# Performance work log

Hardware: AMD Instinct MI355X
Metric: run time of the kernel (lower is better)

Reference implementation:

```python
import jax, jax.numpy as jnp
import numpy as np

B, S, E, H, FF = 4, 2048, 1024, 16, 4096
TD = 32  # transition_dim


def _layer_norm(v, g, b, eps=1e-5):
    m = v.mean(-1, keepdims=True)
    var = ((v - m) ** 2).mean(-1, keepdims=True)
    return (v - m) * jax.lax.rsqrt(var + eps) * g + b


def setup_inputs() -> dict:
    key = jax.random.key(0)
    ks = jax.random.split(key, 8)
    w = 0.02
    return {
        "x": jax.random.normal(ks[0], (B, S, E), dtype=jnp.float32),
        "transition_dim": TD,
        "ln1_g": jnp.ones((E,), jnp.float32),
        "ln1_b": jnp.zeros((E,), jnp.float32),
        "ln2_g": jnp.ones((E,), jnp.float32),
        "ln2_b": jnp.zeros((E,), jnp.float32),
        "w_qkv": jax.random.normal(ks[1], (3 * E, E), jnp.float32) * w,
        "b_qkv": jnp.zeros((3 * E,), jnp.float32),
        "w_o": jax.random.normal(ks[2], (E, E), jnp.float32) * w,
        "b_o": jnp.zeros((E,), jnp.float32),
        "w_fc1": jax.random.normal(ks[3], (FF, E), jnp.float32) * w,
        "b_fc1": jnp.zeros((FF,), jnp.float32),
        "w_fc2": jax.random.normal(ks[4], (E, FF), jnp.float32) * w,
        "b_fc2": jnp.zeros((E,), jnp.float32),
    }


def reference(x, transition_dim, ln1_g, ln1_b, ln2_g, ln2_b, w_qkv, b_qkv,
              w_o, b_o, w_fc1, b_fc1, w_fc2, b_fc2):
    Bx, Sx, Ex = x.shape
    Dh = Ex // H
    xn = _layer_norm(x, ln1_g, ln1_b)
    qkv = xn @ w_qkv.T + b_qkv                      # [B,S,3E]
    q, k, v = jnp.split(qkv, 3, axis=-1)
    def heads(t):
        return t.reshape(Bx, Sx, H, Dh).transpose(0, 2, 1, 3)  # [B,H,S,Dh]
    q, k, v = heads(q), heads(k), heads(v)
    scores = jnp.einsum("bhqd,bhkd->bhqk", q, k) / np.sqrt(Dh).astype(np.float32)
    # custom mask: causal (j > i) OR periodic value-column (j % TD == TD-1) blocked
    i = jnp.arange(Sx)
    mask = (i[None, :] > i[:, None]) | ((i[None, :] % transition_dim) == transition_dim - 1)
    scores = jnp.where(mask[None, None], -jnp.inf, scores)
    p = jax.nn.softmax(scores, axis=-1)
    attn = jnp.einsum("bhqk,bhkd->bhqd", p, v)
    attn = attn.transpose(0, 2, 1, 3).reshape(Bx, Sx, Ex)
    attn = attn @ w_o.T + b_o
    x = x + attn
    h = _layer_norm(x, ln2_g, ln2_b)
    h = jax.nn.gelu(h @ w_fc1.T + b_fc1, approximate=False) @ w_fc2.T + b_fc2
    return x + h
```

## Files before the change

kernel.cpp:

```cpp
#include <hip/hip_runtime.h>
#include <hip/hip_bf16.h>

typedef unsigned short u16;
typedef unsigned int u32;
typedef short bf16x8 __attribute__((ext_vector_type(8)));
typedef float f32x4 __attribute__((ext_vector_type(4)));
typedef float f32x16 __attribute__((ext_vector_type(16)));

#define B_ 4
#define S_ 2048
#define E_ 1024
#define H_ 16
#define FF_ 4096
#define M_ 8192

__device__ __forceinline__ u16 f2bf(float f) {
    u32 u = __float_as_uint(f);
    u32 r = (u + 0x7FFFu + ((u >> 16) & 1u)) >> 16;
    return (u16)r;
}
__device__ __forceinline__ float bf2f(u16 v) {
    return __uint_as_float(((u32)v) << 16);
}
__device__ __forceinline__ u32 cvtpk(float lo, float hi) {
    u32 r;
    asm("v_cvt_pk_bf16_f32 %0, %1, %2" : "=v"(r) : "v"(lo), "v"(hi));
    return r;
}
__device__ __forceinline__ void pswap(u32& a, u32& b) {
    asm("v_permlane32_swap_b32 %0, %1" : "+v"(a), "+v"(b));
}
__device__ __forceinline__ void gload16(const void* g, void* l) {
    __builtin_amdgcn_global_load_lds(
        (__attribute__((address_space(1))) void*)g,
        (__attribute__((address_space(3))) void*)l, 16, 0, 0);
}
__device__ __forceinline__ float gelu_f(float v) {
    float y = 0.79788456f * (v + 0.044715f * v * v * v);
    float t = __builtin_amdgcn_exp2f(2.88539008f * y);
    float th = 1.0f - 2.0f / (t + 1.0f);
    return 0.5f * v * (1.0f + th);
}

__global__ __launch_bounds__(256) void cvt4_kernel(const float* __restrict__ s0, u16* __restrict__ d0,
                                                   const float* __restrict__ s1, u16* __restrict__ d1,
                                                   const float* __restrict__ s2, u16* __restrict__ d2,
                                                   const float* __restrict__ s3, u16* __restrict__ d3) {
    int blk = blockIdx.x;
    const float* s; u16* d; int base;
    if (blk < 3072)      { s = s0; d = d0; base = blk; }
    else if (blk < 4096) { s = s1; d = d1; base = blk - 3072; }
    else if (blk < 8192) { s = s2; d = d2; base = blk - 4096; }
    else                 { s = s3; d = d3; base = blk - 8192; }
    int i = base * 256 + threadIdx.x;
    float4 v = ((const float4*)s)[i];
    ushort4 o;
    o.x = f2bf(v.x); o.y = f2bf(v.y); o.z = f2bf(v.z); o.w = f2bf(v.w);
    ((ushort4*)d)[i] = o;
}

__global__ __launch_bounds__(256) void vtrans_kernel(const u16* __restrict__ qkv,
                                                     u16* __restrict__ vt) {
    __shared__ u16 tile[64 * 67];
    int t = threadIdx.x;
    int st = blockIdx.x;
    int bh = blockIdx.y;
    int b = bh >> 4, h = bh & 15;
    int s0 = st * 64;
    int r = t >> 3, c0 = (t & 7) * 8;
#pragma unroll
    for (int half = 0; half < 2; half++) {
        int rr = r + half * 32;
        const u16* src = qkv + (size_t)(b * S_ + s0 + rr) * 3072 + 2048 + h * 64 + c0;
        uint4 v = *(const uint4*)src;
        u16* pv = (u16*)&v;
#pragma unroll
        for (int e = 0; e < 8; e++) tile[(c0 + e) * 67 + rr] = pv[e];
    }
    __syncthreads();
    int d = t >> 2, ch = t & 3;
    u16 buf[16];
#pragma unroll
    for (int j = 0; j < 16; j++) buf[j] = tile[d * 67 + ch * 16 + j];
    u16* dst = vt + ((size_t)bh * 64 + d) * 2048 + s0 + ch * 16;
    *(uint4*)dst = *(uint4*)&buf[0];
    *(uint4*)(dst + 8) = *(uint4*)&buf[8];
}

__global__ __launch_bounds__(256) void ln_kernel(const float* __restrict__ x,
                                                 const float* __restrict__ g,
                                                 const float* __restrict__ bb,
                                                 u16* __restrict__ out) {
    int row = blockIdx.x;
    int t = threadIdx.x;
    const float4* xr = (const float4*)(x + (size_t)row * E_);
    float4 v = xr[t];
    float s = v.x + v.y + v.z + v.w;
    float sq = v.x * v.x + v.y * v.y + v.z * v.z + v.w * v.w;
    for (int o = 1; o < 64; o <<= 1) {
        s += __shfl_xor(s, o, 64);
        sq += __shfl_xor(sq, o, 64);
    }
    __shared__ float ss[4], sqs[4];
    int w = t >> 6, l = t & 63;
    if (l == 0) { ss[w] = s; sqs[w] = sq; }
    __syncthreads();
    s = ss[0] + ss[1] + ss[2] + ss[3];
    sq = sqs[0] + sqs[1] + sqs[2] + sqs[3];
    float mean = s * (1.0f / E_);
    float var = sq * (1.0f / E_) - mean * mean;
    float rstd = rsqrtf(var + 1e-5f);
    float4 gv = ((const float4*)g)[t];
    float4 bv = ((const float4*)bb)[t];
    ushort4 o4;
    o4.x = f2bf((v.x - mean) * rstd * gv.x + bv.x);
    o4.y = f2bf((v.y - mean) * rstd * gv.y + bv.y);
    o4.z = f2bf((v.z - mean) * rstd * gv.z + bv.z);
    o4.w = f2bf((v.w - mean) * rstd * gv.w + bv.w);
    ((ushort4*)(out + (size_t)row * E_))[t] = o4;
}

__global__ __launch_bounds__(256) void ln_bf16_kernel(const u16* __restrict__ x,
                                                      const float* __restrict__ g,
                                                      const float* __restrict__ bb,
                                                      u16* __restrict__ out) {
    int row = blockIdx.x;
    int t = threadIdx.x;
    ushort4 xv = ((const ushort4*)(x + (size_t)row * E_))[t];
    float v0 = bf2f(xv.x), v1 = bf2f(xv.y), v2 = bf2f(xv.z), v3 = bf2f(xv.w);
    float s = v0 + v1 + v2 + v3;
    float sq = v0 * v0 + v1 * v1 + v2 * v2 + v3 * v3;
    for (int o = 1; o < 64; o <<= 1) {
        s += __shfl_xor(s, o, 64);
        sq += __shfl_xor(sq, o, 64);
    }
    __shared__ float ss[4], sqs[4];
    int w = t >> 6, l = t & 63;
    if (l == 0) { ss[w] = s; sqs[w] = sq; }
    __syncthreads();
    s = ss[0] + ss[1] + ss[2] + ss[3];
    sq = sqs[0] + sqs[1] + sqs[2] + sqs[3];
    float mean = s * (1.0f / E_);
    float var = sq * (1.0f / E_) - mean * mean;
    float rstd = rsqrtf(var + 1e-5f);
    float4 gv = ((const float4*)g)[t];
    float4 bv = ((const float4*)bb)[t];
    ushort4 o4;
    o4.x = f2bf((v0 - mean) * rstd * gv.x + bv.x);
    o4.y = f2bf((v1 - mean) * rstd * gv.y + bv.y);
    o4.z = f2bf((v2 - mean) * rstd * gv.z + bv.z);
    o4.w = f2bf((v3 - mean) * rstd * gv.w + bv.w);
    ((ushort4*)(out + (size_t)row * E_))[t] = o4;
}

template <int EPI>
__global__ __launch_bounds__(512) void gemm256m(const u16* __restrict__ A,
                                                const u16* __restrict__ Bt,
                                                const float* __restrict__ bias,
                                                void* __restrict__ outp,
                                                int N, int K) {
    __shared__ u16 ldsA[2 * 2 * 8192];
    __shared__ u16 ldsB[2 * 2 * 8192];
    int t = threadIdx.x;
    int wid = t >> 6, l = t & 63, l15 = l & 15, hi4 = l >> 4;
    int wm = wid >> 2, wn = wid & 3;

    int nwg = gridDim.x;
    int flat = blockIdx.x;
    int swz = (flat & 7) * (nwg >> 3) + (flat >> 3);
    int nx = N >> 8;
    int nxs = nx >> 2;
    int sid = swz >> 4, wi = swz & 15;
    int sidm = sid / nxs, sidn = sid % nxs;
    int m0 = (sidm * 4 + (wi >> 2)) * 256;
    int n0 = (sidn * 4 + (wi & 3)) * 256;
    const size_t Kb = (size_t)K * 2;

    f32x4 acc[8][4];
    f32x4 zf = {0.f, 0.f, 0.f, 0.f};
#pragma unroll
    for (int i = 0; i < 8; i++)
#pragma unroll
        for (int j = 0; j < 4; j++) acc[i][j] = zf;

    auto stageA = [&](int buf, int h, int k0) {
#pragma unroll
        for (int rr = 0; rr < 2; ++rr) {
            int o = t * 16 + rr * 8192;
            int lr = o >> 7;
            int gch = ((o >> 4) & 7) ^ (lr & 7);
            int grow = m0 + (lr >> 6) * 128 + h * 64 + (lr & 63);
            gload16((const char*)A + (size_t)grow * Kb + k0 * 2 + gch * 16,
                    (char*)ldsA + (buf * 2 + h) * 16384 + o);
        }
    };
    auto stageB = [&](int buf, int h, int k0) {
#pragma unroll
        for (int rr = 0; rr < 2; ++rr) {
            int o = t * 16 + rr * 8192;
            int lr = o >> 7;
            int gch = ((o >> 4) & 7) ^ (lr & 7);
            int grow = n0 + (lr >> 5) * 64 + h * 32 + (lr & 31);
            gload16((const char*)Bt + (size_t)grow * Kb + k0 * 2 + gch * 16,
                    (char*)ldsB + (buf * 2 + h) * 16384 + o);
        }
    };

    auto readA = [&](int bq, int mh, bf16x8 (&af)[4][2]) {
#pragma unroll
        for (int mi = 0; mi < 4; mi++)
#pragma unroll
            for (int ks = 0; ks < 2; ks++) {
                int lr = wm * 64 + mi * 16 + l15;
                int ob = lr * 128 + ks * 64 + hi4 * 16;
                af[mi][ks] = *(const bf16x8*)((const char*)ldsA +
                             (bq * 2 + mh) * 16384 + (ob ^ ((lr & 7) << 4)));
            }
    };
    auto readB = [&](int bq, int nh, bf16x8 (&bfr)[2][2]) {
#pragma unroll
        for (int nq = 0; nq < 2; nq++)
#pragma unroll
            for (int ks = 0; ks < 2; ks++) {
                int lr = wn * 32 + nq * 16 + l15;
                int ob = lr * 128 + ks * 64 + hi4 * 16;
                bfr[nq][ks] = *(const bf16x8*)((const char*)ldsB +
                              (bq * 2 + nh) * 16384 + (ob ^ ((lr & 7) << 4)));
            }
    };
    auto mma = [&](bf16x8 (&af)[4][2], bf16x8 (&bfr)[2][2], int mh, int nh) {
#pragma unroll
        for (int mi = 0; mi < 4; mi++)
#pragma unroll
            for (int nq = 0; nq < 2; nq++)
#pragma unroll
                for (int ks = 0; ks < 2; ks++)
                    acc[mh * 4 + mi][nh * 2 + nq] =
                        __builtin_amdgcn_mfma_f32_16x16x32_bf16(
                            af[mi][ks], bfr[nq][ks], acc[mh * 4 + mi][nh * 2 + nq], 0, 0, 0);
    };

#define GWAIT(N)                                            \
    asm volatile("s_waitcnt vmcnt(" #N ")" ::: "memory");   \
    __builtin_amdgcn_sched_barrier(0);
#define PH_MID                                              \
    __builtin_amdgcn_s_barrier();                           \
    asm volatile("s_waitcnt lgkmcnt(0)" ::: "memory");      \
    __builtin_amdgcn_sched_barrier(0);                      \
    __builtin_amdgcn_s_setprio(1);
#define PH_END                                              \
    __builtin_amdgcn_s_setprio(0);                          \
    __builtin_amdgcn_s_barrier();

    int ITERS = K >> 7;
    stageB(0, 0, 0); stageB(0, 1, 0); stageA(0, 0, 0); stageA(0, 1, 0);
    stageB(1, 0, 64); stageB(1, 1, 64); stageA(1, 0, 64);
    GWAIT(6);
    __builtin_amdgcn_s_barrier();
    for (int s = 0; s < ITERS; ++s) {
        int k1 = (2 * s + 1) << 6;
        int k2 = (2 * s + 2) << 6; if (k2 >= K) k2 = 0;
        int k3 = (2 * s + 3) << 6; if (k3 >= K) k3 = 0;
        bf16x8 af[4][2], b0[2][2], b1[2][2];
        readA(0, 0, af); readB(0, 0, b0); readB(0, 1, b1);
        stageA(1, 1, k1);
        PH_MID; mma(af, b0, 0, 0); mma(af, b1, 0, 1); PH_END;
        readA(0, 1, af);
        stageB(0, 0, k2); stageB(0, 1, k2); stageA(0, 0, k2);
        PH_MID; mma(af, b0, 1, 0); mma(af, b1, 1, 1);
        __builtin_amdgcn_s_setprio(0);
        GWAIT(8);
        __builtin_amdgcn_s_barrier();
        readA(1, 0, af); readB(1, 0, b0); readB(1, 1, b1);
        stageA(0, 1, k2);
        PH_MID; mma(af, b0, 0, 0); mma(af, b1, 0, 1);
        __builtin_amdgcn_s_setprio(0);
        GWAIT(8);
        __builtin_amdgcn_s_barrier();
        readA(1, 1, af);
        stageB(1, 0, k3); stageB(1, 1, k3); stageA(1, 0, k3);
        GWAIT(6);
        PH_MID; mma(af, b0, 1, 0); mma(af, b1, 1, 1); PH_END;
    }
    GWAIT(0);
    __builtin_amdgcn_s_barrier();
#undef GWAIT
#undef PH_MID
#undef PH_END

    float bias_v[4];
#pragma unroll
    for (int nf = 0; nf < 4; nf++) bias_v[nf] = bias[n0 + wn * 64 + nf * 16 + l15];

    u16* myl = (wid < 4 ? ldsA : ldsB) + (wid & 3) * 8192;
#pragma unroll
    for (int mf = 0; mf < 8; mf++)
#pragma unroll
        for (int nf = 0; nf < 4; nf++)
#pragma unroll
            for (int j = 0; j < 4; j++) {
                int row = mf * 16 + hi4 * 4 + j;
                int col = nf * 16 + l15;
                float v = acc[mf][nf][j] + bias_v[nf];
                if (EPI == 2) v = gelu_f(v);
                int chunk = ((col >> 3) + (row >> 2)) & 7;
                myl[row * 64 + chunk * 8 + (col & 7)] = f2bf(v);
            }
    u16* out16 = (u16*)outp;
#pragma unroll
    for (int pass = 0; pass < 16; ++pass) {
        int row = pass * 8 + (l >> 3);
        int chunk = ((l & 7) + (row >> 2)) & 7;
        uint4 d = *(const uint4*)&myl[row * 64 + chunk * 8];
        int grow = m0 + wm * 128 + row;
        int gcol = n0 + wn * 64 + (l & 7) * 8;
        *(uint4*)&out16[(size_t)grow * N + gcol] = d;
    }
}

template <int EPI>
__global__ __launch_bounds__(512) void gemm256n128(const u16* __restrict__ A,
                                                   const u16* __restrict__ Bt,
                                                   const float* __restrict__ bias,
                                                   void* __restrict__ outp,
                                                   const void* __restrict__ residp,
                                                   int N, int K) {
    __shared__ u16 ldsA[2 * 2 * 8192];
    __shared__ u16 ldsB[2 * 8192];
    int t = threadIdx.x;
    int wid = t >> 6, l = t & 63, l15 = l & 15, hi4 = l >> 4;
    int wm = wid >> 2, wn = wid & 3;

    int nwg = gridDim.x;
    int flat = blockIdx.x;
    int swz = (flat & 7) * (nwg >> 3) + (flat >> 3);
    int nx = N >> 7;
    int nxs = nx >> 2;
    int sid = swz >> 4, wi = swz & 15;
    int sidm = sid / nxs, sidn = sid % nxs;
    int m0 = (sidm * 4 + (wi >> 2)) * 256;
    int n0 = (sidn * 4 + (wi & 3)) * 128;
    const size_t Kb = (size_t)K * 2;

    f32x4 acc[8][2];
    f32x4 zf = {0.f, 0.f, 0.f, 0.f};
#pragma unroll
    for (int i = 0; i < 8; i++)
#pragma unroll
        for (int j = 0; j < 2; j++) acc[i][j] = zf;

    auto stageA = [&](int buf, int h, int k0) {
#pragma unroll
        for (int rr = 0; rr < 2; ++rr) {
            int o = t * 16 + rr * 8192;
            int lr = o >> 7;
            int gch = ((o >> 4) & 7) ^ (lr & 7);
            int grow = m0 + (lr >> 6) * 128 + h * 64 + (lr & 63);
            gload16((const char*)A + (size_t)grow * Kb + k0 * 2 + gch * 16,
                    (char*)ldsA + (buf * 2 + h) * 16384 + o);
        }
    };
    auto stageB = [&](int buf, int k0) {
#pragma unroll
        for (int rr = 0; rr < 2; ++rr) {
            int o = t * 16 + rr * 8192;
            int lr = o >> 7;
            int gch = ((o >> 4) & 7) ^ (lr & 7);
            int grow = n0 + lr;
            gload16((const char*)Bt + (size_t)grow * Kb + k0 * 2 + gch * 16,
                    (char*)ldsB + buf * 16384 + o);
        }
    };

    auto readA = [&](int bq, int mh, bf16x8 (&af)[4][2]) {
#pragma unroll
        for (int mi = 0; mi < 4; mi++)
#pragma unroll
            for (int ks = 0; ks < 2; ks++) {
                int lr = wm * 64 + mi * 16 + l15;
                int ob = lr * 128 + ks * 64 + hi4 * 16;
                af[mi][ks] = *(const bf16x8*)((const char*)ldsA +
                             (bq * 2 + mh) * 16384 + (ob ^ ((lr & 7) << 4)));
            }
    };
    auto readB = [&](int bq, bf16x8 (&bfr)[2][2]) {
#pragma unroll
        for (int nq = 0; nq < 2; nq++)
#pragma unroll
            for (int ks = 0; ks < 2; ks++) {
                int lr = wn * 32 + nq * 16 + l15;
                int ob = lr * 128 + ks * 64 + hi4 * 16;
                bfr[nq][ks] = *(const bf16x8*)((const char*)ldsB +
                              bq * 16384 + (ob ^ ((lr & 7) << 4)));
            }
    };
    auto mma = [&](bf16x8 (&af)[4][2], bf16x8 (&bfr)[2][2], int mh) {
#pragma unroll
        for (int mi = 0; mi < 4; mi++)
#pragma unroll
            for (int nq = 0; nq < 2; nq++)
#pragma unroll
                for (int ks = 0; ks < 2; ks++)
                    acc[mh * 4 + mi][nq] =
                        __builtin_amdgcn_mfma_f32_16x16x32_bf16(
                            af[mi][ks], bfr[nq][ks], acc[mh * 4 + mi][nq], 0, 0, 0);
    };

#define GWAIT(N)                                            \
    asm volatile("s_waitcnt vmcnt(" #N ")" ::: "memory");   \
    __builtin_amdgcn_sched_barrier(0);
#define PH_MID                                              \
    __builtin_amdgcn_s_barrier();                           \
    asm volatile("s_waitcnt lgkmcnt(0)" ::: "memory");      \
    __builtin_amdgcn_sched_barrier(0);                      \
    __builtin_amdgcn_s_setprio(1);
#define PH_END                                              \
    __builtin_amdgcn_s_setprio(0);                          \
    __builtin_amdgcn_s_barrier();

    int ITERS = K >> 7;
    stageB(0, 0); stageA(0, 0, 0); stageA(0, 1, 0);
    stageB(1, 64); stageA(1, 0, 64);
    GWAIT(4);
    __builtin_amdgcn_s_barrier();
    for (int s = 0; s < ITERS; ++s) {
        int k1 = (2 * s + 1) << 6;
        int k2 = (2 * s + 2) << 6; if (k2 >= K) k2 = 0;
        int k3 = (2 * s + 3) << 6; if (k3 >= K) k3 = 0;
        bf16x8 af[4][2], br[2][2];
        readA(0, 0, af); readB(0, br); stageA(1, 1, k1);
        PH_MID; mma(af, br, 0); PH_END;
        readA(0, 1, af); stageB(0, k2); stageA(0, 0, k2); GWAIT(4);
        PH_MID; mma(af, br, 1); PH_END;
        readA(1, 0, af); readB(1, br); stageA(0, 1, k2);
        PH_MID; mma(af, br, 0); PH_END;
        readA(1, 1, af); stageB(1, k3); stageA(1, 0, k3); GWAIT(4);
        PH_MID; mma(af, br, 1); PH_END;
    }
    GWAIT(0);
#undef GWAIT
#undef PH_MID
#undef PH_END

    float bias_v[2];
#pragma unroll
    for (int nq = 0; nq < 2; nq++) bias_v[nq] = bias[n0 + wn * 32 + nq * 16 + l15];

    if constexpr (EPI == 0 || EPI == 3) {
        __builtin_amdgcn_s_barrier();
        u16* myl = ldsA + wid * 4096;
        const float* resf = (const float*)residp;
#pragma unroll
        for (int mf = 0; mf < 8; mf++)
#pragma unroll
            for (int nq = 0; nq < 2; nq++)
#pragma unroll
                for (int j = 0; j < 4; j++) {
                    int row = mf * 16 + hi4 * 4 + j;
                    int col = nq * 16 + l15;
                    float v = acc[mf][nq][j] + bias_v[nq];
                    if (EPI == 3)
                        v += resf[(size_t)(m0 + wm * 128 + row) * N + (n0 + wn * 32 + col)];
                    int chunk = ((col >> 3) + (row >> 2)) & 3;
                    myl[row * 32 + chunk * 8 + (col & 7)] = f2bf(v);
                }
        u16* out16 = (u16*)outp;
#pragma unroll
        for (int pass = 0; pass < 8; ++pass) {
            int row = pass * 16 + (l >> 2);
            int cc = l & 3;
            int chunk = (cc + (row >> 2)) & 3;
            uint4 d = *(const uint4*)&myl[row * 32 + chunk * 8];
            int grow = m0 + wm * 128 + row;
            int gcol = n0 + wn * 32 + cc * 8;
            *(uint4*)&out16[(size_t)grow * N + gcol] = d;
        }
    } else {
        const u16* res16 = (const u16*)residp;
#pragma unroll
        for (int mf = 0; mf < 8; mf++)
#pragma unroll
            for (int nq = 0; nq < 2; nq++)
#pragma unroll
                for (int j = 0; j < 4; j++) {
                    int row = m0 + wm * 128 + mf * 16 + hi4 * 4 + j;
                    int col = n0 + wn * 32 + nq * 16 + l15;
                    size_t idx = (size_t)row * N + col;
                    float v = acc[mf][nq][j] + bias_v[nq] + bf2f(res16[idx]);
                    ((float*)outp)[idx] = v;
                }
    }
}

__global__ __launch_bounds__(128) void attn_kernel(const u16* __restrict__ qkv,
                                                   const u16* __restrict__ vt,
                                                   u16* __restrict__ aout) {
    __shared__ u16 Ksb[2 * 4096];
    __shared__ u16 Vsb[2 * 4096];
    int t = threadIdx.x;
    int wv = t >> 6, l = t & 63;
    int q31 = l & 31, hi = l >> 5;
    int flat = blockIdx.x;
    int logical = (flat & 7) * 128 + (flat >> 3);
    int bh = logical >> 4, p0 = logical & 15;
    int b = bh >> 4, h = bh & 15;

    const float qs = 0.18033688011f;

    const char* srcK0 = (const char*)(qkv + E_ + (size_t)(b * S_ + (t >> 3)) * 3072 + h * 64) +
                        ((t & 7) ^ ((t >> 3) & 7)) * 16;
    const char* srcV0 = (const char*)(vt + ((size_t)(bh * 64 + (t >> 3))) * 2048) +
                        ((t & 7) ^ ((t >> 3) & 7)) * 16;
    auto issueK = [&](int buf, int j0) {
#pragma unroll
        for (int pp = 0; pp < 4; pp++)
            gload16(srcK0 + (size_t)pp * 98304 + (size_t)j0 * 6144,
                    (char*)Ksb + buf * 8192 + 16 * t + 2048 * pp);
    };
    auto issueV = [&](int buf, int j0) {
#pragma unroll
        for (int pp = 0; pp < 4; pp++)
            gload16(srcV0 + (size_t)pp * 65536 + (size_t)j0 * 2,
                    (char*)Vsb + buf * 8192 + 16 * t + 2048 * pp);
    };

    f32x16 zf16;
#pragma unroll
    for (int r = 0; r < 16; r++) zf16[r] = 0.f;

    for (int half = 0; half < 2; ++half) {
        int qt = half ? (31 - p0) : p0;
        int rowq = qt * 64 + wv * 32 + q31;

        bf16x8 qreg[4];
        const u16* qbase = qkv + (size_t)(b * S_ + rowq) * 3072 + h * 64 + hi * 8;
#pragma unroll
        for (int g = 0; g < 4; g++) {
            uint4 d16 = *(const uint4*)(qbase + 16 * g);
            u32 uu[4] = {d16.x, d16.y, d16.z, d16.w};
            bf16x8 qv;
#pragma unroll
            for (int e = 0; e < 8; e++) {
                u16 raw = (e & 1) ? (u16)(uu[e >> 1] >> 16) : (u16)(uu[e >> 1] & 0xffffu);
                qv[e] = (short)f2bf(bf2f(raw) * qs);
            }
            qreg[g] = qv;
        }

        f32x16 o0 = zf16, o1 = zf16;
        float lrun = 0.f;

        int j1 = (qt >= 1) ? 64 : 0;
        issueK(0, 0); issueV(0, 0);
        issueK(1, j1); issueV(1, j1);

        for (int jt = 0; jt <= qt; ++jt) {
            int cur = jt & 1;
            int j0 = jt * 64;
            asm volatile("s_waitcnt vmcnt(8)" ::: "memory");
            __builtin_amdgcn_sched_barrier(0);
            __builtin_amdgcn_s_barrier();

            const u16* Kc = Ksb + cur * 4096;
            const u16* Vc = Vsb + cur * 4096;

            f32x16 s0 = zf16, s1 = zf16;
            __builtin_amdgcn_s_setprio(1);
#pragma unroll
            for (int g = 0; g < 4; g++) {
                int r0 = q31, r1 = 32 + q31;
                bf16x8 k0 = *(const bf16x8*)&Kc[((r0 << 6) + hi * 8 + 16 * g) ^ ((r0 & 7) << 3)];
                bf16x8 k1 = *(const bf16x8*)&Kc[((r1 << 6) + hi * 8 + 16 * g) ^ ((r1 & 7) << 3)];
                s0 = __builtin_amdgcn_mfma_f32_32x32x16_bf16(k0, qreg[g], s0, 0, 0, 0);
                s1 = __builtin_amdgcn_mfma_f32_32x32x16_bf16(k1, qreg[g], s1, 0, 0, 0);
            }
            __builtin_amdgcn_s_setprio(0);

            int cb0 = j0 + 4 * hi;
            float sa = 0.f, sb = 0.f, sc2 = 0.f, sd = 0.f;
            if (jt == qt) {
#pragma unroll
                for (int r = 0; r < 16; r++) {
                    const int cc = (r & 3) + 8 * (r >> 2);
                    bool bad0 = (cb0 + cc > rowq) || (r == 15 && hi);
                    bool bad1 = (cb0 + 32 + cc > rowq) || (r == 15 && hi);
                    float p0 = bad0 ? 0.f : __builtin_amdgcn_exp2f(s0[r]);
                    float p1 = bad1 ? 0.f : __builtin_amdgcn_exp2f(s1[r]);
                    s0[r] = p0; s1[r] = p1;
                    if (r & 1) { sb += p0; sd += p1; } else { sa += p0; sc2 += p1; }
                }
            } else {
#pragma unroll
                for (int r = 0; r < 16; r++) {
                    float p0 = __builtin_amdgcn_exp2f(s0[r]);
                    float p1 = __builtin_amdgcn_exp2f(s1[r]);
                    if (r == 15 && hi) { p0 = 0.f; p1 = 0.f; }
                    s0[r] = p0; s1[r] = p1;
                    if (r & 1) { sb += p0; sd += p1; } else { sa += p0; sc2 += p1; }
                }
            }
            lrun += (sa + sb) + (sc2 + sd);

            bf16x8 pa[4];
#pragma unroll
            for (int g = 0; g < 4; g++) {
                const int bs = (g & 1) * 8;
                u32 wa, wb, wc, wd;
                if (g < 2) {
                    wa = cvtpk(s0[bs + 0], s0[bs + 1]);
                    wb = cvtpk(s0[bs + 4], s0[bs + 5]);
                    wc = cvtpk(s0[bs + 2], s0[bs + 3]);
                    wd = cvtpk(s0[bs + 6], s0[bs + 7]);
                } else {
                    wa = cvtpk(s1[bs + 0], s1[bs + 1]);
                    wb = cvtpk(s1[bs + 4], s1[bs + 5]);
                    wc = cvtpk(s1[bs + 2], s1[bs + 3]);
                    wd = cvtpk(s1[bs + 6], s1[bs + 7]);
                }
                pswap(wa, wb);
                pswap(wc, wd);
                union { u32 w[4]; bf16x8 f; } u;
                u.w[0] = wa; u.w[1] = wc; u.w[2] = wb; u.w[3] = wd;
                pa[g] = u.f;
            }

            __builtin_amdgcn_s_setprio(1);
#pragma unroll
            for (int g = 0; g < 4; g++) {
                int d0 = q31, d1 = 32 + q31;
                bf16x8 v0 = *(const bf16x8*)&Vc[((d0 << 6) + hi * 8 + 16 * g) ^ ((d0 & 7) << 3)];
                bf16x8 v1 = *(const bf16x8*)&Vc[((d1 << 6) + hi * 8 + 16 * g) ^ ((d1 & 7) << 3)];
                o0 = __builtin_amdgcn_mfma_f32_32x32x16_bf16(v0, pa[g], o0, 0, 0, 0);
                o1 = __builtin_amdgcn_mfma_f32_32x32x16_bf16(v1, pa[g], o1, 0, 0, 0);
            }
            __builtin_amdgcn_s_setprio(0);

            __builtin_amdgcn_s_barrier();
            int nj = (jt + 2 <= qt) ? (jt + 2) * 64 : 0;
            issueK(cur, nj);
            issueV(cur, nj);
        }

        lrun += __shfl_xor(lrun, 32, 64);
        float inv = 1.0f / lrun;
        u16* orow = aout + (size_t)(b * S_ + rowq) * E_ + h * 64 + 4 * hi;
#pragma unroll
        for (int r = 0; r < 16; r++) {
            const int cc = (r & 3) + 8 * (r >> 2);
            orow[cc] = f2bf(o0[r] * inv);
            orow[32 + cc] = f2bf(o1[r] * inv);
        }

        if (half == 0) {
            asm volatile("s_waitcnt vmcnt(0)" ::: "memory");
            __builtin_amdgcn_sched_barrier(0);
            __builtin_amdgcn_s_barrier();
        }
    }
}

extern "C" void kernel_launch(void* const* d_in, const int* in_sizes, int n_in,
                              void* d_out, int out_size, void* d_ws, size_t ws_size,
                              hipStream_t stream) {
    const float* x = (const float*)d_in[0];
    const float* ln1_g = (const float*)d_in[2];
    const float* ln1_b = (const float*)d_in[3];
    const float* ln2_g = (const float*)d_in[4];
    const float* ln2_b = (const float*)d_in[5];
    const float* w_qkv = (const float*)d_in[6];
    const float* b_qkv = (const float*)d_in[7];
    const float* w_o = (const float*)d_in[8];
    const float* b_o = (const float*)d_in[9];
    const float* w_fc1 = (const float*)d_in[10];
    const float* b_fc1 = (const float*)d_in[11];
    const float* w_fc2 = (const float*)d_in[12];
    const float* b_fc2 = (const float*)d_in[13];
    float* out = (float*)d_out;
    char* ws = (char*)d_ws;

    u16* wqkv_bf = (u16*)(ws);
    u16* wo_bf   = (u16*)(ws + 6291456);
    u16* wfc1_bf = (u16*)(ws + 8388608);
    u16* wfc2_bf = (u16*)(ws + 16777216);
    u16* xn_bf   = (u16*)(ws + 25165824);
    u16* qkv_bf  = (u16*)(ws + 41943040);
    u16* ffn1_bf = (u16*)(ws + 41943040);
    u16* attn_bf = (u16*)(ws + 92274688);
    u16* vtw     = (u16*)(ws + 109051904);
    u16* x2b     = (u16*)(ws + 125829120);
    (void)in_sizes; (void)n_in; (void)out_size; (void)ws_size;

    cvt4_kernel<<<12288, 256, 0, stream>>>(w_qkv, wqkv_bf, w_o, wo_bf,
                                           w_fc1, wfc1_bf, w_fc2, wfc2_bf);

    ln_kernel<<<M_, 256, 0, stream>>>(x, ln1_g, ln1_b, xn_bf);

    gemm256n128<0><<<768, 512, 0, stream>>>(xn_bf, wqkv_bf, b_qkv, qkv_bf, nullptr, 3072, 1024);

    vtrans_kernel<<<dim3(32, 64), 256, 0, stream>>>(qkv_bf, vtw);

    attn_kernel<<<1024, 128, 0, stream>>>(qkv_bf, vtw, attn_bf);

    gemm256n128<3><<<256, 512, 0, stream>>>(attn_bf, wo_bf, b_o, x2b, x, 1024, 1024);

    ln_bf16_kernel<<<M_, 256, 0, stream>>>(x2b, ln2_g, ln2_b, xn_bf);

    gemm256m<2><<<512, 512, 0, stream>>>(xn_bf, wfc1_bf, b_fc1, ffn1_bf, 4096, 1024);

    gemm256n128<4><<<256, 512, 0, stream>>>(ffn1_bf, wfc2_bf, b_fc2, out, x2b, 1024, 4096);
}
```

Before: 355.1 us.

## Grow attention query tile to 128 rows with four waves per block

The attention kernel now runs 256 threads (four waves) per block, each block covering a 128-row query tile, with half as many blocks. Each K/V tile loaded into shared memory is reused by twice as many query rows, so global-to-LDS traffic per unit of work drops, and each thread issues two loads per tile instead of four. Waves whose rows lie entirely before a key tile skip its compute, but they still take part in the barriers. This adds causal-diagonal imbalance inside a block, and the grid is coarser, with 512 blocks instead of 1024.

```diff
diff --git a/kernel.cpp b/kernel.cpp
--- a/kernel.cpp
+++ b/kernel.cpp
@@ -492,7 +492,7 @@
     }
 }
 
-__global__ __launch_bounds__(128) void attn_kernel(const u16* __restrict__ qkv,
+__global__ __launch_bounds__(256) void attn_kernel(const u16* __restrict__ qkv,
                                                    const u16* __restrict__ vt,
                                                    u16* __restrict__ aout) {
     __shared__ u16 Ksb[2 * 4096];
@@ -501,27 +501,24 @@
     int wv = t >> 6, l = t & 63;
     int q31 = l & 31, hi = l >> 5;
     int flat = blockIdx.x;
-    int logical = (flat & 7) * 128 + (flat >> 3);
-    int bh = logical >> 4, p0 = logical & 15;
+    int logical = (flat & 7) * 64 + (flat >> 3);
+    int bh = logical >> 3, p0 = logical & 7;
     int b = bh >> 4, h = bh & 15;
 
     const float qs = 0.18033688011f;
 
-    const char* srcK0 = (const char*)(qkv + E_ + (size_t)(b * S_ + (t >> 3)) * 3072 + h * 64) +
-                        ((t & 7) ^ ((t >> 3) & 7)) * 16;
-    const char* srcV0 = (const char*)(vt + ((size_t)(bh * 64 + (t >> 3))) * 2048) +
-                        ((t & 7) ^ ((t >> 3) & 7)) * 16;
+    int row0 = t >> 3, ch0 = t & 7;
+    int gch0 = ch0 ^ (row0 & 7);
+    const char* srcK0 = (const char*)(qkv + E_ + (size_t)(b * S_ + row0) * 3072 + h * 64) + gch0 * 16;
+    const char* srcV0 = (const char*)(vt + ((size_t)(bh * 64 + row0)) * 2048) + gch0 * 16;
+
     auto issueK = [&](int buf, int j0) {
-#pragma unroll
-        for (int pp = 0; pp < 4; pp++)
-            gload16(srcK0 + (size_t)pp * 98304 + (size_t)j0 * 6144,
-                    (char*)Ksb + buf * 8192 + 16 * t + 2048 * pp);
+        gload16(srcK0 + (size_t)j0 * 6144, (char*)Ksb + buf * 8192 + t * 16);
+        gload16(srcK0 + (size_t)j0 * 6144 + 32 * 6144, (char*)Ksb + buf * 8192 + t * 16 + 4096);
     };
     auto issueV = [&](int buf, int j0) {
-#pragma unroll
-        for (int pp = 0; pp < 4; pp++)
-            gload16(srcV0 + (size_t)pp * 65536 + (size_t)j0 * 2,
-                    (char*)Vsb + buf * 8192 + 16 * t + 2048 * pp);
+        gload16(srcV0 + (size_t)j0 * 2, (char*)Vsb + buf * 8192 + t * 16);
+        gload16(srcV0 + (size_t)j0 * 2 + 32 * 4096, (char*)Vsb + buf * 8192 + t * 16 + 4096);
     };
 
     f32x16 zf16;
@@ -529,8 +526,9 @@
     for (int r = 0; r < 16; r++) zf16[r] = 0.f;
 
     for (int half = 0; half < 2; ++half) {
-        int qt = half ? (31 - p0) : p0;
-        int rowq = qt * 64 + wv * 32 + q31;
+        int qt = half ? (15 - p0) : p0;
+        int wrow_min = qt * 128 + wv * 32;
+        int rowq = wrow_min + q31;
 
         bf16x8 qreg[4];
         const u16* qbase = qkv + (size_t)(b * S_ + rowq) * 3072 + h * 64 + hi * 8;
@@ -550,93 +548,95 @@
         f32x16 o0 = zf16, o1 = zf16;
         float lrun = 0.f;
 
-        int j1 = (qt >= 1) ? 64 : 0;
+        int ntiles = 2 * qt + 2;
         issueK(0, 0); issueV(0, 0);
-        issueK(1, j1); issueV(1, j1);
-
-        for (int jt = 0; jt <= qt; ++jt) {
+        issueK(1, 64); issueV(1, 64);
+
+        for (int jt = 0; jt < ntiles; ++jt) {
             int cur = jt & 1;
             int j0 = jt * 64;
-            asm volatile("s_waitcnt vmcnt(8)" ::: "memory");
+            asm volatile("s_waitcnt vmcnt(4)" ::: "memory");
             __builtin_amdgcn_sched_barrier(0);
             __builtin_amdgcn_s_barrier();
 
-            const u16* Kc = Ksb + cur * 4096;
-            const u16* Vc = Vsb + cur * 4096;
-
-            f32x16 s0 = zf16, s1 = zf16;
-            __builtin_amdgcn_s_setprio(1);
-#pragma unroll
-            for (int g = 0; g < 4; g++) {
-                int r0 = q31, r1 = 32 + q31;
-                bf16x8 k0 = *(const bf16x8*)&Kc[((r0 << 6) + hi * 8 + 16 * g) ^ ((r0 & 7) << 3)];
-                bf16x8 k1 = *(const bf16x8*)&Kc[((r1 << 6) + hi * 8 + 16 * g) ^ ((r1 & 7) << 3)];
-                s0 = __builtin_amdgcn_mfma_f32_32x32x16_bf16(k0, qreg[g], s0, 0, 0, 0);
-                s1 = __builtin_amdgcn_mfma_f32_32x32x16_bf16(k1, qreg[g], s1, 0, 0, 0);
+            if (j0 <= wrow_min + 31) {
+                const u16* Kc = Ksb + cur * 4096;
+                const u16* Vc = Vsb + cur * 4096;
+
+                f32x16 s0 = zf16, s1 = zf16;
+                __builtin_amdgcn_s_setprio(1);
+#pragma unroll
+                for (int g = 0; g < 4; g++) {
+                    int r0 = q31, r1 = 32 + q31;
+                    bf16x8 k0 = *(const bf16x8*)&Kc[((r0 << 6) + hi * 8 + 16 * g) ^ ((r0 & 7) << 3)];
+                    bf16x8 k1 = *(const bf16x8*)&Kc[((r1 << 6) + hi * 8 + 16 * g) ^ ((r1 & 7) << 3)];
+                    s0 = __builtin_amdgcn_mfma_f32_32x32x16_bf16(k0, qreg[g], s0, 0, 0, 0);
+                    s1 = __builtin_amdgcn_mfma_f32_32x32x16_bf16(k1, qreg[g], s1, 0, 0, 0);
+                }
+                __builtin_amdgcn_s_setprio(0);
+
+                int cb0 = j0 + 4 * hi;
+                float sa = 0.f, sb = 0.f, sc2 = 0.f, sd = 0.f;
+                if (j0 + 63 > wrow_min) {
+#pragma unroll
+                    for (int r = 0; r < 16; r++) {
+                        const int cc = (r & 3) + 8 * (r >> 2);
+                        bool bad0 = (cb0 + cc > rowq) || (r == 15 && hi);
+                        bool bad1 = (cb0 + 32 + cc > rowq) || (r == 15 && hi);
+                        float p0 = bad0 ? 0.f : __builtin_amdgcn_exp2f(s0[r]);
+                        float p1 = bad1 ? 0.f : __builtin_amdgcn_exp2f(s1[r]);
+                        s0[r] = p0; s1[r] = p1;
+                        if (r & 1) { sb += p0; sd += p1; } else { sa += p0; sc2 += p1; }
+                    }
+                } else {
+#pragma unroll
+                    for (int r = 0; r < 16; r++) {
+                        float p0 = __builtin_amdgcn_exp2f(s0[r]);
+                        float p1 = __builtin_amdgcn_exp2f(s1[r]);
+                        if (r == 15 && hi) { p0 = 0.f; p1 = 0.f; }
+                        s0[r] = p0; s1[r] = p1;
+                        if (r & 1) { sb += p0; sd += p1; } else { sa += p0; sc2 += p1; }
+                    }
+                }
+                lrun += (sa + sb) + (sc2 + sd);
+
+                bf16x8 pa[4];
+#pragma unroll
+                for (int g = 0; g < 4; g++) {
+                    const int bs = (g & 1) * 8;
+                    u32 wa, wb, wc, wd;
+                    if (g < 2) {
+                        wa = cvtpk(s0[bs + 0], s0[bs + 1]);
+                        wb = cvtpk(s0[bs + 4], s0[bs + 5]);
+                        wc = cvtpk(s0[bs + 2], s0[bs + 3]);
+                        wd = cvtpk(s0[bs + 6], s0[bs + 7]);
+                    } else {
+                        wa = cvtpk(s1[bs + 0], s1[bs + 1]);
+                        wb = cvtpk(s1[bs + 4], s1[bs + 5]);
+                        wc = cvtpk(s1[bs + 2], s1[bs + 3]);
+                        wd = cvtpk(s1[bs + 6], s1[bs + 7]);
+                    }
+                    pswap(wa, wb);
+                    pswap(wc, wd);
+                    union { u32 w[4]; bf16x8 f; } u;
+                    u.w[0] = wa; u.w[1] = wc; u.w[2] = wb; u.w[3] = wd;
+                    pa[g] = u.f;
+                }
+
+                __builtin_amdgcn_s_setprio(1);
+#pragma unroll
+                for (int g = 0; g < 4; g++) {
+                    int d0 = q31, d1 = 32 + q31;
+                    bf16x8 v0 = *(const bf16x8*)&Vc[((d0 << 6) + hi * 8 + 16 * g) ^ ((d0 & 7) << 3)];
+                    bf16x8 v1 = *(const bf16x8*)&Vc[((d1 << 6) + hi * 8 + 16 * g) ^ ((d1 & 7) << 3)];
+                    o0 = __builtin_amdgcn_mfma_f32_32x32x16_bf16(v0, pa[g], o0, 0, 0, 0);
+                    o1 = __builtin_amdgcn_mfma_f32_32x32x16_bf16(v1, pa[g], o1, 0, 0, 0);
+                }
+                __builtin_amdgcn_s_setprio(0);
             }
-            __builtin_amdgcn_s_setprio(0);
-
-            int cb0 = j0 + 4 * hi;
-            float sa = 0.f, sb = 0.f, sc2 = 0.f, sd = 0.f;
-            if (jt == qt) {
-#pragma unroll
-                for (int r = 0; r < 16; r++) {
-                    const int cc = (r & 3) + 8 * (r >> 2);
-                    bool bad0 = (cb0 + cc > rowq) || (r == 15 && hi);
-                    bool bad1 = (cb0 + 32 + cc > rowq) || (r == 15 && hi);
-                    float p0 = bad0 ? 0.f : __builtin_amdgcn_exp2f(s0[r]);
-                    float p1 = bad1 ? 0.f : __builtin_amdgcn_exp2f(s1[r]);
-                    s0[r] = p0; s1[r] = p1;
-                    if (r & 1) { sb += p0; sd += p1; } else { sa += p0; sc2 += p1; }
-                }
-            } else {
-#pragma unroll
-                for (int r = 0; r < 16; r++) {
-                    float p0 = __builtin_amdgcn_exp2f(s0[r]);
-                    float p1 = __builtin_amdgcn_exp2f(s1[r]);
-                    if (r == 15 && hi) { p0 = 0.f; p1 = 0.f; }
-                    s0[r] = p0; s1[r] = p1;
-                    if (r & 1) { sb += p0; sd += p1; } else { sa += p0; sc2 += p1; }
-                }
-            }
-            lrun += (sa + sb) + (sc2 + sd);
-
-            bf16x8 pa[4];
-#pragma unroll
-            for (int g = 0; g < 4; g++) {
-                const int bs = (g & 1) * 8;
-                u32 wa, wb, wc, wd;
-                if (g < 2) {
-                    wa = cvtpk(s0[bs + 0], s0[bs + 1]);
-                    wb = cvtpk(s0[bs + 4], s0[bs + 5]);
-                    wc = cvtpk(s0[bs + 2], s0[bs + 3]);
-                    wd = cvtpk(s0[bs + 6], s0[bs + 7]);
-                } else {
-                    wa = cvtpk(s1[bs + 0], s1[bs + 1]);
-                    wb = cvtpk(s1[bs + 4], s1[bs + 5]);
-                    wc = cvtpk(s1[bs + 2], s1[bs + 3]);
-                    wd = cvtpk(s1[bs + 6], s1[bs + 7]);
-                }
-                pswap(wa, wb);
-                pswap(wc, wd);
-                union { u32 w[4]; bf16x8 f; } u;
-                u.w[0] = wa; u.w[1] = wc; u.w[2] = wb; u.w[3] = wd;
-                pa[g] = u.f;
-            }
-
-            __builtin_amdgcn_s_setprio(1);
-#pragma unroll
-            for (int g = 0; g < 4; g++) {
-                int d0 = q31, d1 = 32 + q31;
-                bf16x8 v0 = *(const bf16x8*)&Vc[((d0 << 6) + hi * 8 + 16 * g) ^ ((d0 & 7) << 3)];
-                bf16x8 v1 = *(const bf16x8*)&Vc[((d1 << 6) + hi * 8 + 16 * g) ^ ((d1 & 7) << 3)];
-                o0 = __builtin_amdgcn_mfma_f32_32x32x16_bf16(v0, pa[g], o0, 0, 0, 0);
-                o1 = __builtin_amdgcn_mfma_f32_32x32x16_bf16(v1, pa[g], o1, 0, 0, 0);
-            }
-            __builtin_amdgcn_s_setprio(0);
 
             __builtin_amdgcn_s_barrier();
-            int nj = (jt + 2 <= qt) ? (jt + 2) * 64 : 0;
+            int nj = (jt + 2 < ntiles) ? (jt + 2) * 64 : 0;
             issueK(cur, nj);
             issueV(cur, nj);
         }
@@ -699,7 +699,7 @@
 
     vtrans_kernel<<<dim3(32, 64), 256, 0, stream>>>(qkv_bf, vtw);
 
-    attn_kernel<<<1024, 128, 0, stream>>>(qkv_bf, vtw, attn_bf);
+    attn_kernel<<<512, 256, 0, stream>>>(qkv_bf, vtw, attn_bf);
 
     gemm256n128<3><<<256, 512, 0, stream>>>(attn_bf, wo_bf, b_o, x2b, x, 1024, 1024);
 
```

New measurement: 347.2 us (median of 2 runs). 1.02x faster.
